# Optimization experiments

Hardware: AMD Instinct MI355X
Metric: run time of the kernel (lower is better)

The kernel has to match this reference:

```python
import jax, jax.numpy as jnp
import numpy as np

MIN_AREA, MAX_AREA = 0.001, 0.5
MAX_COMPONENTS = 10.0
MAX_PERIMETER_RATIO = 100.0
EPS = 1e-6


def setup_inputs() -> dict:
    key = jax.random.key(0)
    masks = jax.random.normal(key, (128, 1024, 1024), dtype=jnp.float32)
    return {"masks": masks}


def reference(masks):
    # masks: (N, H, W) logits. sigmoid(x) > 0.5  <=>  x > 0
    dt = masks.dtype
    binary = (masks > 0).astype(dt)  # (N, H, W)
    N, H, W = binary.shape
    total_pixels = jnp.asarray(H * W, dt)

    # 3x3 ring kernel (center 0), same padding -> neighbor count per pixel
    kernel = jnp.array([[1, 1, 1], [1, 0, 1], [1, 1, 1]], dtype=dt).reshape(1, 1, 3, 3)
    neighbor_sum = jax.lax.conv_general_dilated(
        binary[:, None, :, :], kernel, window_strides=(1, 1), padding='SAME')[:, 0]  # (N,H,W)

    area = binary.sum(axis=(1, 2))  # (N,)
    area_ratio = area / total_pixels
    area_score = jnp.where((area_ratio >= MIN_AREA) & (area_ratio <= MAX_AREA), 1.0, 0.1)

    connectivity = (neighbor_sum * binary).sum(axis=(1, 2))  # (N,)
    safe_area = jnp.where(area > 0, area, 1.0)
    component_score = jnp.where(
        connectivity > 0,
        jnp.minimum(1.0, MAX_COMPONENTS / (connectivity / safe_area + EPS)),
        0.1,
    )

    perimeter = jnp.maximum(neighbor_sum - 4.0 * binary, 0.0).sum(axis=(1, 2))  # (N,)
    par = perimeter / safe_area
    shape_score = jnp.where(
        area > 0,
        jnp.where(par <= MAX_PERIMETER_RATIO, 1.0,
                  jnp.maximum(0.1, MAX_PERIMETER_RATIO / (par + EPS))),
        0.1,
    )

    validity = 0.4 * area_score + 0.3 * component_score + 0.3 * shape_score
    return jnp.maximum(jnp.asarray(0.05, dt), validity.astype(dt))
```

## Files before the change

### kernel.cpp

```cpp
#include <hip/hip_runtime.h>


#define N_IMG 128
#define H 1024
#define W 1024
#define CHUNKS 16
#define ROWS (H / CHUNKS)
#define NPART (N_IMG * CHUNKS)

__global__ __launch_bounds__(256, 8) void dasp_sums_kernel(
    const float* __restrict__ masks, unsigned int* __restrict__ partials) {
    const int blk = blockIdx.x;
    const int img = blk / CHUNKS;
    const int chunk = blk - img * CHUNKS;
    const int r0 = chunk * ROWS;
    const int r1 = r0 + ROWS;

    const int wave = threadIdx.x >> 6;
    const int lane = threadIdx.x & 63;
    const int col0 = wave * 256 + lane * 4;

    const float* base = masks + (size_t)img * H * W;

    const bool isL = (lane == 0);
    const bool isR = (lane == 63);
    const int hcol = isL ? (col0 - 1) : (col0 + 4);
    const bool hvalid = (isL || isR) && (hcol >= 0) && (hcol < W);

    auto fetch = [&](int y, float4& f, float& hf) {
        f = make_float4(0.f, 0.f, 0.f, 0.f);
        hf = 0.f;
        if (y >= 0 && y < H) {
            f = *reinterpret_cast<const float4*>(base + (size_t)y * W + col0);
            if (hvalid) hf = base[(size_t)y * W + hcol];
        }
    };

    float4 fp, fc, fn;
    float hfp, hfc, hfn;
    fetch(r0 - 1, fp, hfp);
    fetch(r0, fc, hfc);
    fetch(r0 + 1, fn, hfn);

    int bp0 = fp.x > 0.f, bp1 = fp.y > 0.f, bp2 = fp.z > 0.f, bp3 = fp.w > 0.f;
    int bc0 = fc.x > 0.f, bc1 = fc.y > 0.f, bc2 = fc.z > 0.f, bc3 = fc.w > 0.f;
    int hp = hfp > 0.f, hc = hfc > 0.f;

    int area = 0, conn = 0, per = 0;

    for (int y = r0; y < r1; ++y) {
        float4 f2;
        float hf2;
        const int y2 = y + 2;
        if (y2 <= r1) {
            fetch(y2, f2, hf2);
        } else {
            f2 = make_float4(0.f, 0.f, 0.f, 0.f);
            hf2 = 0.f;
        }

        const int bn0 = fn.x > 0.f, bn1 = fn.y > 0.f, bn2 = fn.z > 0.f,
                  bn3 = fn.w > 0.f;
        const int hn = hfn > 0.f;

        const int c0 = bp0 + bc0 + bn0;
        const int c1 = bp1 + bc1 + bn1;
        const int c2 = bp2 + bc2 + bn2;
        const int c3 = bp3 + bc3 + bn3;
        const int ch = hp + hc + hn;

        int cl = __shfl_up(c3, 1);
        int cr = __shfl_down(c0, 1);
        if (isL) cl = ch;
        if (isR) cr = ch;

        const int n0 = cl + c0 + c1 - bc0;
        const int n1 = c0 + c1 + c2 - bc1;
        const int n2 = c1 + c2 + c3 - bc2;
        const int n3 = c2 + c3 + cr - bc3;

        area += bc0 + bc1 + bc2 + bc3;
        conn += n0 * bc0 + n1 * bc1 + n2 * bc2 + n3 * bc3;
        per += max(n0 - 4 * bc0, 0) + max(n1 - 4 * bc1, 0) +
               max(n2 - 4 * bc2, 0) + max(n3 - 4 * bc3, 0);

        bp0 = bc0; bp1 = bc1; bp2 = bc2; bp3 = bc3;
        bc0 = bn0; bc1 = bn1; bc2 = bn2; bc3 = bn3;
        hp = hc; hc = hn;
        fn = f2; hfn = hf2;
    }

    #pragma unroll
    for (int m = 32; m >= 1; m >>= 1) {
        area += __shfl_xor(area, m);
        conn += __shfl_xor(conn, m);
        per += __shfl_xor(per, m);
    }

    __shared__ int sA[4], sC[4], sP[4];
    if (lane == 0) {
        sA[wave] = area;
        sC[wave] = conn;
        sP[wave] = per;
    }
    __syncthreads();
    if (threadIdx.x == 0) {
        const unsigned int a = (unsigned)(sA[0] + sA[1] + sA[2] + sA[3]);
        const unsigned int c = (unsigned)(sC[0] + sC[1] + sC[2] + sC[3]);
        const unsigned int p = (unsigned)(sP[0] + sP[1] + sP[2] + sP[3]);
        partials[blk] = a;
        partials[NPART + blk] = c;
        partials[2 * NPART + blk] = p;
    }
}

__global__ void dasp_score_kernel(const unsigned int* __restrict__ partials,
                                  float* __restrict__ out) {
    const int n = threadIdx.x;
    if (n >= N_IMG) return;
    unsigned int a = 0, c = 0, p = 0;
    #pragma unroll
    for (int k = 0; k < CHUNKS; ++k) {
        a += partials[n * CHUNKS + k];
        c += partials[NPART + n * CHUNKS + k];
        p += partials[2 * NPART + n * CHUNKS + k];
    }
    const float areaf = (float)a;
    const float ratio = areaf / (float)(H * W);
    const float area_score = (ratio >= 0.001f && ratio <= 0.5f) ? 1.0f : 0.1f;
    const float safe = (a > 0) ? areaf : 1.0f;
    const float connf = (float)c;
    const float comp =
        (c > 0) ? fminf(1.0f, 10.0f / (connf / safe + 1e-6f)) : 0.1f;
    const float perf = (float)p;
    const float par = perf / safe;
    const float shape =
        (a > 0) ? ((par <= 100.0f) ? 1.0f
                                   : fmaxf(0.1f, 100.0f / (par + 1e-6f)))
                : 0.1f;
    const float v = 0.4f * area_score + 0.3f * comp + 0.3f * shape;
    out[n] = fmaxf(0.05f, v);
}

extern "C" void kernel_launch(void* const* d_in, const int* in_sizes, int n_in,
                              void* d_out, int out_size, void* d_ws,
                              size_t ws_size, hipStream_t stream) {
    const float* masks = (const float*)d_in[0];
    float* out = (float*)d_out;
    unsigned int* partials = (unsigned int*)d_ws;

    dasp_sums_kernel<<<dim3(N_IMG * CHUNKS), dim3(256), 0, stream>>>(masks,
                                                                     partials);
    dasp_score_kernel<<<dim3(1), dim3(128), 0, stream>>>(partials, out);
}
```

Before: 678.2 us.

## Pack binary pixels into bytes and accumulate stats with SAD instructions per wave

Each wave now owns a full-width 32-row strip. Each lane loads four float4 segments per row, and a two-row prefetch is kept in flight. Binary pixels are packed four per 32-bit word so the vertical and horizontal neighbour sums run as byte-SIMD integer adds, with cross-lane shuffles providing the halo bytes. Area, connectivity and perimeter are accumulated with v_sad_u8, and perimeter is derived as (|n-4b| + n - 4b)/2. This cuts ALU work and the halo scalar loads, at the cost of more registers (launch bounds lowered to 4), 64 halo rows per image instead of 16, and a dependence on byte lanes not overflowing.

```diff
diff --git a/kernel.cpp b/kernel.cpp
--- a/kernel.cpp
+++ b/kernel.cpp
@@ -4,126 +4,169 @@
 #define N_IMG 128
 #define H 1024
 #define W 1024
-#define CHUNKS 16
-#define ROWS (H / CHUNKS)
-#define NPART (N_IMG * CHUNKS)
+#define WROWS 32
+#define WAVES_PER_BLOCK 4
+#define BROWS (WROWS * WAVES_PER_BLOCK)
+#define BLOCKS_PER_IMG (H / BROWS)
+#define NPART (N_IMG * BLOCKS_PER_IMG)
 
-__global__ __launch_bounds__(256, 8) void dasp_sums_kernel(
-    const float* __restrict__ masks, unsigned int* __restrict__ partials) {
+static __device__ __forceinline__ unsigned sad8(unsigned a, unsigned b,
+                                                unsigned c) {
+#if __has_builtin(__builtin_amdgcn_sad_u8)
+    return __builtin_amdgcn_sad_u8(a, b, c);
+#else
+    unsigned s = c;
+#pragma unroll
+    for (int k = 0; k < 4; ++k) {
+        unsigned x = (a >> (8 * k)) & 0xFFu, y = (b >> (8 * k)) & 0xFFu;
+        s += (x > y) ? (x - y) : (y - x);
+    }
+    return s;
+#endif
+}
+
+__global__ __launch_bounds__(256, 4) void dasp_sums_kernel(
+    const float* __restrict__ masks, unsigned* __restrict__ partials) {
     const int blk = blockIdx.x;
-    const int img = blk / CHUNKS;
-    const int chunk = blk - img * CHUNKS;
-    const int r0 = chunk * ROWS;
-    const int r1 = r0 + ROWS;
-
+    const int img = blk / BLOCKS_PER_IMG;
+    const int chunk = blk - img * BLOCKS_PER_IMG;
     const int wave = threadIdx.x >> 6;
     const int lane = threadIdx.x & 63;
-    const int col0 = wave * 256 + lane * 4;
 
-    const float* base = masks + (size_t)img * H * W;
+    const int y0 = chunk * BROWS + wave * WROWS;
+    const int yEnd = y0 + WROWS;
 
-    const bool isL = (lane == 0);
-    const bool isR = (lane == 63);
-    const int hcol = isL ? (col0 - 1) : (col0 + 4);
-    const bool hvalid = (isL || isR) && (hcol >= 0) && (hcol < W);
+    const float* __restrict__ base = masks + (size_t)img * (H * W);
 
-    auto fetch = [&](int y, float4& f, float& hf) {
-        f = make_float4(0.f, 0.f, 0.f, 0.f);
-        hf = 0.f;
+    auto fetchRow = [&](int y, float4* f) {
         if (y >= 0 && y < H) {
-            f = *reinterpret_cast<const float4*>(base + (size_t)y * W + col0);
-            if (hvalid) hf = base[(size_t)y * W + hcol];
+            const float* row = base + (size_t)y * W + lane * 4;
+            f[0] = *reinterpret_cast<const float4*>(row);
+            f[1] = *reinterpret_cast<const float4*>(row + 256);
+            f[2] = *reinterpret_cast<const float4*>(row + 512);
+            f[3] = *reinterpret_cast<const float4*>(row + 768);
+        } else {
+            f[0] = f[1] = f[2] = f[3] = make_float4(0.f, 0.f, 0.f, 0.f);
         }
     };
 
-    float4 fp, fc, fn;
-    float hfp, hfc, hfn;
-    fetch(r0 - 1, fp, hfp);
-    fetch(r0, fc, hfc);
-    fetch(r0 + 1, fn, hfn);
+    auto packRow = [&](const float4* f, unsigned* b) {
+#pragma unroll
+        for (int s = 0; s < 4; ++s) {
+            unsigned v = (f[s].x > 0.f) ? 0x00000001u : 0u;
+            v |= (f[s].y > 0.f) ? 0x00000100u : 0u;
+            v |= (f[s].z > 0.f) ? 0x00010000u : 0u;
+            v |= (f[s].w > 0.f) ? 0x01000000u : 0u;
+            b[s] = v;
+        }
+    };
 
-    int bp0 = fp.x > 0.f, bp1 = fp.y > 0.f, bp2 = fp.z > 0.f, bp3 = fp.w > 0.f;
-    int bc0 = fc.x > 0.f, bc1 = fc.y > 0.f, bc2 = fc.z > 0.f, bc3 = fc.w > 0.f;
-    int hp = hfp > 0.f, hc = hfc > 0.f;
+    unsigned bp[4], bc[4];
+    float4 fa[4], fb[4];
+    {
+        float4 t[4];
+        fetchRow(y0 - 1, t);
+        packRow(t, bp);
+        fetchRow(y0, t);
+        packRow(t, bc);
+    }
+    fetchRow(y0 + 1, fa);
+    fetchRow(y0 + 2, fb);
 
-    int area = 0, conn = 0, per = 0;
+    const bool isL0 = (lane == 0);
+    const bool isL63 = (lane == 63);
 
-    for (int y = r0; y < r1; ++y) {
-        float4 f2;
-        float hf2;
-        const int y2 = y + 2;
-        if (y2 <= r1) {
-            fetch(y2, f2, hf2);
+    unsigned area = 0, conn = 0, A1 = 0, A2 = 0;
+
+#pragma unroll 2
+    for (int y = y0; y < yEnd; ++y) {
+        float4 fnew[4];
+        if (y + 3 <= yEnd) {
+            fetchRow(y + 3, fnew);
         } else {
-            f2 = make_float4(0.f, 0.f, 0.f, 0.f);
-            hf2 = 0.f;
+            fnew[0] = fnew[1] = fnew[2] = fnew[3] =
+                make_float4(0.f, 0.f, 0.f, 0.f);
         }
 
-        const int bn0 = fn.x > 0.f, bn1 = fn.y > 0.f, bn2 = fn.z > 0.f,
-                  bn3 = fn.w > 0.f;
-        const int hn = hfn > 0.f;
+        unsigned bn[4];
+        packRow(fa, bn);
 
-        const int c0 = bp0 + bc0 + bn0;
-        const int c1 = bp1 + bc1 + bn1;
-        const int c2 = bp2 + bc2 + bn2;
-        const int c3 = bp3 + bc3 + bn3;
-        const int ch = hp + hc + hn;
+        unsigned c[4];
+#pragma unroll
+        for (int s = 0; s < 4; ++s) c[s] = bp[s] + bc[s] + bn[s];
 
-        int cl = __shfl_up(c3, 1);
-        int cr = __shfl_down(c0, 1);
-        if (isL) cl = ch;
-        if (isR) cr = ch;
+#pragma unroll
+        for (int s = 0; s < 4; ++s) {
+            unsigned cls = __shfl_up(c[s], 1);
+            const unsigned bcl = (s > 0) ? __shfl(c[s - 1], 63) : 0u;
+            cls = isL0 ? bcl : cls;
+            unsigned crs = __shfl_down(c[s], 1);
+            const unsigned bcr = (s < 3) ? __shfl(c[s + 1], 0) : 0u;
+            crs = isL63 ? bcr : crs;
 
-        const int n0 = cl + c0 + c1 - bc0;
-        const int n1 = c0 + c1 + c2 - bc1;
-        const int n2 = c1 + c2 + c3 - bc2;
-        const int n3 = c2 + c3 + cr - bc3;
+            const unsigned left = (c[s] << 8) | (cls >> 24);
+            const unsigned right = (c[s] >> 8) | (crs << 24);
+            const unsigned n = c[s] + left + right - bc[s];
 
-        area += bc0 + bc1 + bc2 + bc3;
-        conn += n0 * bc0 + n1 * bc1 + n2 * bc2 + n3 * bc3;
-        per += max(n0 - 4 * bc0, 0) + max(n1 - 4 * bc1, 0) +
-               max(n2 - 4 * bc2, 0) + max(n3 - 4 * bc3, 0);
+            const unsigned bmask = (bc[s] << 8) - bc[s];
+            area = sad8(bc[s], 0u, area);
+            A2 = sad8(n, 0u, A2);
+            A1 = sad8(n, bc[s] << 2, A1);
+            conn = sad8(n & bmask, 0u, conn);
+        }
 
-        bp0 = bc0; bp1 = bc1; bp2 = bc2; bp3 = bc3;
-        bc0 = bn0; bc1 = bn1; bc2 = bn2; bc3 = bn3;
-        hp = hc; hc = hn;
-        fn = f2; hfn = hf2;
+#pragma unroll
+        for (int s = 0; s < 4; ++s) {
+            bp[s] = bc[s];
+            bc[s] = bn[s];
+            fa[s] = fb[s];
+            fb[s] = fnew[s];
+        }
     }
 
-    #pragma unroll
+    int a = (int)area;
+    int cn = (int)conn;
+    int p = (int)((A1 + A2 - 4u * area) >> 1);
+
+#pragma unroll
     for (int m = 32; m >= 1; m >>= 1) {
-        area += __shfl_xor(area, m);
-        conn += __shfl_xor(conn, m);
-        per += __shfl_xor(per, m);
+        a += __shfl_xor(a, m);
+        cn += __shfl_xor(cn, m);
+        p += __shfl_xor(p, m);
     }
 
-    __shared__ int sA[4], sC[4], sP[4];
+    __shared__ int sA[WAVES_PER_BLOCK], sC[WAVES_PER_BLOCK],
+        sP[WAVES_PER_BLOCK];
     if (lane == 0) {
-        sA[wave] = area;
-        sC[wave] = conn;
-        sP[wave] = per;
+        sA[wave] = a;
+        sC[wave] = cn;
+        sP[wave] = p;
     }
     __syncthreads();
     if (threadIdx.x == 0) {
-        const unsigned int a = (unsigned)(sA[0] + sA[1] + sA[2] + sA[3]);
-        const unsigned int c = (unsigned)(sC[0] + sC[1] + sC[2] + sC[3]);
-        const unsigned int p = (unsigned)(sP[0] + sP[1] + sP[2] + sP[3]);
-        partials[blk] = a;
-        partials[NPART + blk] = c;
-        partials[2 * NPART + blk] = p;
+        int ta = 0, tc = 0, tp = 0;
+#pragma unroll
+        for (int wv = 0; wv < WAVES_PER_BLOCK; ++wv) {
+            ta += sA[wv];
+            tc += sC[wv];
+            tp += sP[wv];
+        }
+        partials[blk] = (unsigned)ta;
+        partials[NPART + blk] = (unsigned)tc;
+        partials[2 * NPART + blk] = (unsigned)tp;
     }
 }
 
-__global__ void dasp_score_kernel(const unsigned int* __restrict__ partials,
+__global__ void dasp_score_kernel(const unsigned* __restrict__ partials,
                                   float* __restrict__ out) {
     const int n = threadIdx.x;
     if (n >= N_IMG) return;
-    unsigned int a = 0, c = 0, p = 0;
-    #pragma unroll
-    for (int k = 0; k < CHUNKS; ++k) {
-        a += partials[n * CHUNKS + k];
-        c += partials[NPART + n * CHUNKS + k];
-        p += partials[2 * NPART + n * CHUNKS + k];
+    unsigned a = 0, c = 0, p = 0;
+#pragma unroll
+    for (int k = 0; k < BLOCKS_PER_IMG; ++k) {
+        a += partials[n * BLOCKS_PER_IMG + k];
+        c += partials[NPART + n * BLOCKS_PER_IMG + k];
+        p += partials[2 * NPART + n * BLOCKS_PER_IMG + k];
     }
     const float areaf = (float)a;
     const float ratio = areaf / (float)(H * W);
@@ -135,9 +178,9 @@
     const float perf = (float)p;
     const float par = perf / safe;
     const float shape =
-        (a > 0) ? ((par <= 100.0f) ? 1.0f
-                                   : fmaxf(0.1f, 100.0f / (par + 1e-6f)))
-                : 0.1f;
+        (a > 0)
+            ? ((par <= 100.0f) ? 1.0f : fmaxf(0.1f, 100.0f / (par + 1e-6f)))
+            : 0.1f;
     const float v = 0.4f * area_score + 0.3f * comp + 0.3f * shape;
     out[n] = fmaxf(0.05f, v);
 }
@@ -147,9 +190,9 @@
                               size_t ws_size, hipStream_t stream) {
     const float* masks = (const float*)d_in[0];
     float* out = (float*)d_out;
-    unsigned int* partials = (unsigned int*)d_ws;
+    unsigned* partials = (unsigned*)d_ws;
 
-    dasp_sums_kernel<<<dim3(N_IMG * CHUNKS), dim3(256), 0, stream>>>(masks,
-                                                                     partials);
+    dasp_sums_kernel<<<dim3(N_IMG * BLOCKS_PER_IMG), dim3(256), 0, stream>>>(
+        masks, partials);
     dasp_score_kernel<<<dim3(1), dim3(128), 0, stream>>>(partials, out);
 }
```

Measured after the change: 677.9 us. About the same (-0.0%).
